# Optimization experiments

Hardware: AMD Instinct MI355X
Metric: run time of the kernel (lower is better)

## Reference

```python
import jax, jax.numpy as jnp
import numpy as np

N = 50000      # nodes
E = 800000     # edges (avg degree 16)
IN = 128       # in_channels
OUT = 128      # out_channels


def setup_inputs() -> dict:
    key = jax.random.key(0)
    k1, k2, k3 = jax.random.split(key, 3)
    x = jax.random.normal(k1, (N, IN), dtype=jnp.float32)
    edge_index = jax.random.randint(k2, (2, E), 0, N, dtype=jnp.int32)
    # GCNConv params: glorot-ish linear weight + zero bias
    W = jax.random.normal(k3, (IN, OUT), dtype=jnp.float32) / np.float32(np.sqrt(IN))
    b = jnp.zeros((OUT,), dtype=jnp.float32)
    return {"x": x, "W": W, "b": b, "edge_index": edge_index}


def reference(x, W, b, edge_index):
    n = x.shape[0]
    src, dst = edge_index[0], edge_index[1]
    # add self loops (GCNConv default add_self_loops=True)
    loop = jnp.arange(n, dtype=edge_index.dtype)
    src = jnp.concatenate([src, loop])
    dst = jnp.concatenate([dst, loop])
    # symmetric normalization: deg^{-1/2}[src] * deg^{-1/2}[dst], deg from dst (flow source_to_target)
    deg = jax.ops.segment_sum(jnp.ones_like(dst, dtype=x.dtype), dst, num_segments=n)
    dinv = jnp.where(deg > 0, jax.lax.rsqrt(jnp.maximum(deg, 1.0)), 0.0)
    norm = dinv[src] * dinv[dst]                     # [E+N]
    xw = x @ W                                       # [N, OUT] dense GEMM first (as GCNConv does)
    msg = xw[src] * norm[:, None]                    # [E+N, OUT] gather + scale
    out = jax.ops.segment_sum(msg, dst, num_segments=n)  # scatter-add aggregate
    return out + b
```

## Files before the change

### kernel.cpp

```cpp
#include <hip/hip_runtime.h>


constexpr int CH = 128;
constexpr int CHUNK = 4096;
constexpr int NCMAX = 256;

typedef __attribute__((ext_vector_type(8))) short short8;
typedef __attribute__((ext_vector_type(4))) float f32x4;

static __device__ __forceinline__ ushort f2bf(float f) {
    unsigned u = __float_as_uint(f);
    u += 0x7fff + ((u >> 16) & 1);
    return (ushort)(u >> 16);
}


__global__ __launch_bounds__(256) void hist_kernel(const int* __restrict__ dst,
                                                   int* __restrict__ h, int E, int nc) {
    __shared__ int hh[NCMAX];
    int t = threadIdx.x, b = blockIdx.x;
    for (int i = t; i < nc; i += 256) hh[i] = 0;
    __syncthreads();
    int s = b * CHUNK, e = min(E, s + CHUNK);
    for (int i = s + t; i < e; i += 256) atomicAdd(&hh[dst[i] >> 8], 1);
    __syncthreads();
    for (int i = t; i < nc; i += 256) h[b * nc + i] = hh[i];
}

__global__ __launch_bounds__(256) void colscan_cols(int* __restrict__ h,
        int* __restrict__ coltot, int nblk, int nc) {
    __shared__ int sm[256];
    int i = blockIdx.x;
    int t = threadIdx.x;
    int v = (t < nblk) ? h[t * nc + i] : 0;
    sm[t] = v;
    __syncthreads();
    #pragma unroll
    for (int d = 1; d < 256; d <<= 1) {
        int u = (t >= d) ? sm[t - d] : 0;
        __syncthreads();
        sm[t] += u;
        __syncthreads();
    }
    if (t < nblk) h[t * nc + i] = sm[t] - v;
    if (t == 255) coltot[i] = sm[255];
}

__global__ __launch_bounds__(256) void scan_bbase(const int* __restrict__ coltot,
        int* __restrict__ bbase, int nc) {
    __shared__ int sm[256];
    int t = threadIdx.x;
    int v = (t < nc) ? coltot[t] : 0;
    sm[t] = v;
    __syncthreads();
    #pragma unroll
    for (int d = 1; d < 256; d <<= 1) {
        int u = (t >= d) ? sm[t - d] : 0;
        __syncthreads();
        sm[t] += u;
        __syncthreads();
    }
    if (t < nc) bbase[t] = sm[t] - v;
    if (t == nc - 1) bbase[nc] = sm[t];
}

__global__ __launch_bounds__(256) void binscatter_kernel(const int* __restrict__ src,
        const int* __restrict__ dst, const int* __restrict__ h,
        const int* __restrict__ bbase, uint2* __restrict__ ebuf, int E, int nc) {
    __shared__ int cur[NCMAX];
    int t = threadIdx.x, b = blockIdx.x;
    for (int i = t; i < nc; i += 256) cur[i] = h[b * nc + i] + bbase[i];
    __syncthreads();
    int s = b * CHUNK, e = min(E, s + CHUNK);
    for (int i = s + t; i < e; i += 256) {
        int d = dst[i];
        int pos = atomicAdd(&cur[d >> 8], 1);
        ebuf[pos] = make_uint2((unsigned)src[i], (unsigned)d);
    }
}

__global__ __launch_bounds__(256) void bucket_csr_kernel(const uint2* __restrict__ ebuf,
        const int* __restrict__ bbase, int* __restrict__ off, int* __restrict__ csr,
        float* __restrict__ dinv, int N) {
    __shared__ int hist[256], cur[256], sc[256];
    int t = threadIdx.x, k = blockIdx.x;
    int s = bbase[k], e = bbase[k + 1];
    hist[t] = 0;
    __syncthreads();
    for (int i = s + t; i < e; i += 256) atomicAdd(&hist[ebuf[i].y & 255], 1);
    __syncthreads();
    int v = hist[t];
    sc[t] = v;
    __syncthreads();
    #pragma unroll
    for (int d = 1; d < 256; d <<= 1) {
        int u = (t >= d) ? sc[t - d] : 0;
        __syncthreads();
        sc[t] += u;
        __syncthreads();
    }
    int excl = sc[t] - v;
    int node = k * 256 + t;
    if (node <= N) off[node] = s + excl;
    if (node < N) dinv[node] = rsqrtf((float)(v + 1));
    cur[t] = s + excl;
    __syncthreads();
    for (int i = s + t; i < e; i += 256) {
        uint2 u = ebuf[i];
        int pos = atomicAdd(&cur[u.y & 255], 1);
        csr[pos] = (int)u.x;
    }
}


__global__ void pack_w(const float* __restrict__ W, ushort* __restrict__ Wp) {
    int tid = blockIdx.x * blockDim.x + threadIdx.x;
    if (tid >= 2048) return;
    int col = tid >> 4, chunk = tid & 15;
    ushort tmp[8];
    #pragma unroll
    for (int i = 0; i < 8; ++i)
        tmp[i] = f2bf(W[(size_t)(chunk * 8 + i) * CH + col]);
    int d = col * 16 + (chunk ^ (col & 7));
    *(uint4*)&Wp[(size_t)d * 8] = *(uint4*)tmp;
}


__global__ __launch_bounds__(256) void gemm_mfma(const float* __restrict__ x,
        const ushort* __restrict__ Wp, const float* __restrict__ dinv,
        ushort* __restrict__ xwd, int N) {
    __shared__ alignas(16) ushort Wlds[16384];
    int t = threadIdx.x;
    int wv = t >> 6, l = t & 63;
    int c15 = l & 15, kc = l >> 4;
    int row0 = blockIdx.x * 64 + wv * 16;
    int r = row0 + c15;
    bool valid = r < N;

    short8 af[4];
    #pragma unroll
    for (int ks = 0; ks < 4; ++ks) {
        float4 a0 = make_float4(0.f,0.f,0.f,0.f), a1 = a0;
        if (valid) {
            const float* p = x + (size_t)r * CH + ks * 32 + kc * 8;
            a0 = *(const float4*)p;
            a1 = *(const float4*)(p + 4);
        }
        short8 v;
        v[0]=f2bf(a0.x); v[1]=f2bf(a0.y); v[2]=f2bf(a0.z); v[3]=f2bf(a0.w);
        v[4]=f2bf(a1.x); v[5]=f2bf(a1.y); v[6]=f2bf(a1.z); v[7]=f2bf(a1.w);
        af[ks] = v;
    }

    #pragma unroll
    for (int i = 0; i < 8; ++i) {
        int idx = i * 256 + t;
        *(uint4*)&Wlds[idx * 8] = *(const uint4*)&Wp[idx * 8];
    }
    __syncthreads();

    f32x4 acc[8];
    #pragma unroll
    for (int ct = 0; ct < 8; ++ct) { f32x4 z = {0.f,0.f,0.f,0.f}; acc[ct] = z; }

    int swz = l & 7;
    #pragma unroll
    for (int ks = 0; ks < 4; ++ks) {
        #pragma unroll
        for (int ct = 0; ct < 8; ++ct) {
            int col = ct * 16 + c15;
            int idx16 = (col * 16 + ks * 4 + kc) ^ swz;
            short8 bfrag = *(const short8*)&Wlds[idx16 * 8];
            acc[ct] = __builtin_amdgcn_mfma_f32_16x16x32_bf16(af[ks], bfrag, acc[ct], 0, 0, 0);
        }
    }

    float dv[4];
    #pragma unroll
    for (int rr = 0; rr < 4; ++rr) {
        int row = row0 + kc * 4 + rr;
        dv[rr] = (row < N) ? dinv[row] : 0.f;
    }
    __syncthreads();

    ushort* bw = Wlds + wv * 2048;
    #pragma unroll
    for (int ct = 0; ct < 8; ++ct) {
        #pragma unroll
        for (int rr = 0; rr < 4; ++rr) {
            int row_local = kc * 4 + rr;
            bw[row_local * CH + ct * 16 + c15] = f2bf(acc[ct][rr] * dv[rr]);
        }
    }
    #pragma unroll
    for (int p = 0; p < 4; ++p) {
        int row_local = p * 4 + kc;
        int row = row0 + row_local;
        if (row < N) {
            uint4 vv = *(const uint4*)&bw[row_local * CH + c15 * 8];
            *(uint4*)&xwd[(size_t)row * CH + c15 * 8] = vv;
        }
    }
}


__global__ __launch_bounds__(256) void agg_kernel(const ushort* __restrict__ xwd,
        const int* __restrict__ csr, const int* __restrict__ off,
        const float* __restrict__ dinv, const float* __restrict__ b,
        float* __restrict__ out, int N) {
    int t = threadIdx.x;
    int c15 = t & 15;
    int node = blockIdx.x * 16 + (t >> 4);
    if (node >= N) return;
    int s = off[node], e = off[node + 1];
    float acc[8] = {0.f,0.f,0.f,0.f,0.f,0.f,0.f,0.f};
    const ushort* base = xwd + c15 * 8;

    int sr = (s < e) ? csr[s] : node;
    for (int j = s; j < e; ++j) {
        int nsr = (j + 1 < e) ? csr[j + 1] : node;
        uint4 v = *(const uint4*)(base + (size_t)sr * CH);
        acc[0] += __uint_as_float(v.x << 16);
        acc[1] += __uint_as_float(v.x & 0xffff0000u);
        acc[2] += __uint_as_float(v.y << 16);
        acc[3] += __uint_as_float(v.y & 0xffff0000u);
        acc[4] += __uint_as_float(v.z << 16);
        acc[5] += __uint_as_float(v.z & 0xffff0000u);
        acc[6] += __uint_as_float(v.w << 16);
        acc[7] += __uint_as_float(v.w & 0xffff0000u);
        sr = nsr;
    }
    {
        uint4 v = *(const uint4*)(base + (size_t)node * CH);
        acc[0] += __uint_as_float(v.x << 16);
        acc[1] += __uint_as_float(v.x & 0xffff0000u);
        acc[2] += __uint_as_float(v.y << 16);
        acc[3] += __uint_as_float(v.y & 0xffff0000u);
        acc[4] += __uint_as_float(v.z << 16);
        acc[5] += __uint_as_float(v.z & 0xffff0000u);
        acc[6] += __uint_as_float(v.w << 16);
        acc[7] += __uint_as_float(v.w & 0xffff0000u);
    }
    float di = dinv[node];
    float4 b0 = *(const float4*)&b[c15 * 8];
    float4 b1 = *(const float4*)&b[c15 * 8 + 4];
    float4 o0, o1;
    o0.x = di * acc[0] + b0.x;  o0.y = di * acc[1] + b0.y;
    o0.z = di * acc[2] + b0.z;  o0.w = di * acc[3] + b0.w;
    o1.x = di * acc[4] + b1.x;  o1.y = di * acc[5] + b1.y;
    o1.z = di * acc[6] + b1.z;  o1.w = di * acc[7] + b1.w;
    float* op = out + (size_t)node * CH + c15 * 8;
    *(float4*)op = o0;
    *(float4*)(op + 4) = o1;
}


extern "C" void kernel_launch(void* const* d_in, const int* in_sizes, int n_in,
                              void* d_out, int out_size, void* d_ws, size_t ws_size,
                              hipStream_t stream) {
    const float* x  = (const float*)d_in[0];
    const float* Wm = (const float*)d_in[1];
    const float* b  = (const float*)d_in[2];
    const int*   ei = (const int*)d_in[3];
    int N = in_sizes[0] / CH;
    int E = in_sizes[3] / 2;
    const int* src = ei;
    const int* dst = ei + E;
    float* out = (float*)d_out;

    char* w = (char*)d_ws;
    auto alloc = [&](size_t bytes) {
        char* p = w;
        w += (bytes + 255) & ~(size_t)255;
        return p;
    };
    int nc = (N + 255) >> 8;
    int nblk = (E + CHUNK - 1) / CHUNK;

    ushort* xwd  = (ushort*)alloc((size_t)N * CH * 2);
    uint2*  ebuf = (uint2*)xwd;
    int*    off  = (int*)alloc((size_t)(N + 1) * 4);
    int*    csr  = (int*)alloc((size_t)E * 4);
    float*  dinv = (float*)alloc((size_t)N * 4);
    ushort* Wp   = (ushort*)alloc((size_t)16384 * 2);
    int*    h    = (int*)alloc((size_t)nblk * nc * 4);
    int*    bbase= (int*)alloc((size_t)(nc + 1) * 4);
    int*    coltot=(int*)alloc((size_t)nc * 4);

    hist_kernel<<<nblk, 256, 0, stream>>>(dst, h, E, nc);
    colscan_cols<<<nc, 256, 0, stream>>>(h, coltot, nblk, nc);
    scan_bbase<<<1, 256, 0, stream>>>(coltot, bbase, nc);
    binscatter_kernel<<<nblk, 256, 0, stream>>>(src, dst, h, bbase, ebuf, E, nc);
    bucket_csr_kernel<<<nc, 256, 0, stream>>>(ebuf, bbase, off, csr, dinv, N);
    pack_w<<<8, 256, 0, stream>>>(Wm, Wp);
    gemm_mfma<<<(N + 63) / 64, 256, 0, stream>>>(x, Wp, dinv, xwd, N);
    agg_kernel<<<(N + 15) / 16, 256, 0, stream>>>(xwd, csr, off, dinv, b, out, N);
}
```

Baseline: 95.00 us.

## Pack edge indices into 16 bits and unroll aggregation gather loop by four

```diff
diff --git a/kernel.cpp b/kernel.cpp
--- a/kernel.cpp
+++ b/kernel.cpp
@@ -66,7 +66,7 @@
 
 __global__ __launch_bounds__(256) void binscatter_kernel(const int* __restrict__ src,
         const int* __restrict__ dst, const int* __restrict__ h,
-        const int* __restrict__ bbase, uint2* __restrict__ ebuf, int E, int nc) {
+        const int* __restrict__ bbase, unsigned* __restrict__ ebuf, int E, int nc) {
     __shared__ int cur[NCMAX];
     int t = threadIdx.x, b = blockIdx.x;
     for (int i = t; i < nc; i += 256) cur[i] = h[b * nc + i] + bbase[i];
@@ -75,19 +75,19 @@
     for (int i = s + t; i < e; i += 256) {
         int d = dst[i];
         int pos = atomicAdd(&cur[d >> 8], 1);
-        ebuf[pos] = make_uint2((unsigned)src[i], (unsigned)d);
-    }
-}
-
-__global__ __launch_bounds__(256) void bucket_csr_kernel(const uint2* __restrict__ ebuf,
-        const int* __restrict__ bbase, int* __restrict__ off, int* __restrict__ csr,
+        ebuf[pos] = (unsigned)src[i] | ((unsigned)(d & 255) << 16);
+    }
+}
+
+__global__ __launch_bounds__(256) void bucket_csr_kernel(const unsigned* __restrict__ ebuf,
+        const int* __restrict__ bbase, int* __restrict__ off, ushort* __restrict__ csr,
         float* __restrict__ dinv, int N) {
     __shared__ int hist[256], cur[256], sc[256];
     int t = threadIdx.x, k = blockIdx.x;
     int s = bbase[k], e = bbase[k + 1];
     hist[t] = 0;
     __syncthreads();
-    for (int i = s + t; i < e; i += 256) atomicAdd(&hist[ebuf[i].y & 255], 1);
+    for (int i = s + t; i < e; i += 256) atomicAdd(&hist[(ebuf[i] >> 16) & 255], 1);
     __syncthreads();
     int v = hist[t];
     sc[t] = v;
@@ -106,9 +106,9 @@
     cur[t] = s + excl;
     __syncthreads();
     for (int i = s + t; i < e; i += 256) {
-        uint2 u = ebuf[i];
-        int pos = atomicAdd(&cur[u.y & 255], 1);
-        csr[pos] = (int)u.x;
+        unsigned u = ebuf[i];
+        int pos = atomicAdd(&cur[(u >> 16) & 255], 1);
+        csr[pos] = (ushort)(u & 0xffffu);
     }
 }
 
@@ -204,8 +204,18 @@
 }
 
 
+#define ACC8(v)                                    \
+    acc[0] += __uint_as_float((v).x << 16);        \
+    acc[1] += __uint_as_float((v).x & 0xffff0000u);\
+    acc[2] += __uint_as_float((v).y << 16);        \
+    acc[3] += __uint_as_float((v).y & 0xffff0000u);\
+    acc[4] += __uint_as_float((v).z << 16);        \
+    acc[5] += __uint_as_float((v).z & 0xffff0000u);\
+    acc[6] += __uint_as_float((v).w << 16);        \
+    acc[7] += __uint_as_float((v).w & 0xffff0000u);
+
 __global__ __launch_bounds__(256) void agg_kernel(const ushort* __restrict__ xwd,
-        const int* __restrict__ csr, const int* __restrict__ off,
+        const ushort* __restrict__ csr, const int* __restrict__ off,
         const float* __restrict__ dinv, const float* __restrict__ b,
         float* __restrict__ out, int N) {
     int t = threadIdx.x;
@@ -216,30 +226,23 @@
     float acc[8] = {0.f,0.f,0.f,0.f,0.f,0.f,0.f,0.f};
     const ushort* base = xwd + c15 * 8;
 
-    int sr = (s < e) ? csr[s] : node;
-    for (int j = s; j < e; ++j) {
-        int nsr = (j + 1 < e) ? csr[j + 1] : node;
-        uint4 v = *(const uint4*)(base + (size_t)sr * CH);
-        acc[0] += __uint_as_float(v.x << 16);
-        acc[1] += __uint_as_float(v.x & 0xffff0000u);
-        acc[2] += __uint_as_float(v.y << 16);
-        acc[3] += __uint_as_float(v.y & 0xffff0000u);
-        acc[4] += __uint_as_float(v.z << 16);
-        acc[5] += __uint_as_float(v.z & 0xffff0000u);
-        acc[6] += __uint_as_float(v.w << 16);
-        acc[7] += __uint_as_float(v.w & 0xffff0000u);
-        sr = nsr;
+    int j = s;
+    for (; j + 4 <= e; j += 4) {
+        int i0 = csr[j], i1 = csr[j + 1], i2 = csr[j + 2], i3 = csr[j + 3];
+        uint4 v0 = *(const uint4*)(base + (size_t)i0 * CH);
+        uint4 v1 = *(const uint4*)(base + (size_t)i1 * CH);
+        uint4 v2 = *(const uint4*)(base + (size_t)i2 * CH);
+        uint4 v3 = *(const uint4*)(base + (size_t)i3 * CH);
+        ACC8(v0); ACC8(v1); ACC8(v2); ACC8(v3);
+    }
+    for (; j < e; ++j) {
+        int i0 = csr[j];
+        uint4 v = *(const uint4*)(base + (size_t)i0 * CH);
+        ACC8(v);
     }
     {
         uint4 v = *(const uint4*)(base + (size_t)node * CH);
-        acc[0] += __uint_as_float(v.x << 16);
-        acc[1] += __uint_as_float(v.x & 0xffff0000u);
-        acc[2] += __uint_as_float(v.y << 16);
-        acc[3] += __uint_as_float(v.y & 0xffff0000u);
-        acc[4] += __uint_as_float(v.z << 16);
-        acc[5] += __uint_as_float(v.z & 0xffff0000u);
-        acc[6] += __uint_as_float(v.w << 16);
-        acc[7] += __uint_as_float(v.w & 0xffff0000u);
+        ACC8(v);
     }
     float di = dinv[node];
     float4 b0 = *(const float4*)&b[c15 * 8];
@@ -277,15 +280,15 @@
     int nc = (N + 255) >> 8;
     int nblk = (E + CHUNK - 1) / CHUNK;
 
-    ushort* xwd  = (ushort*)alloc((size_t)N * CH * 2);
-    uint2*  ebuf = (uint2*)xwd;
-    int*    off  = (int*)alloc((size_t)(N + 1) * 4);
-    int*    csr  = (int*)alloc((size_t)E * 4);
-    float*  dinv = (float*)alloc((size_t)N * 4);
-    ushort* Wp   = (ushort*)alloc((size_t)16384 * 2);
-    int*    h    = (int*)alloc((size_t)nblk * nc * 4);
-    int*    bbase= (int*)alloc((size_t)(nc + 1) * 4);
-    int*    coltot=(int*)alloc((size_t)nc * 4);
+    ushort*   xwd  = (ushort*)alloc((size_t)N * CH * 2);
+    unsigned* ebuf = (unsigned*)xwd;
+    int*      off  = (int*)alloc((size_t)(N + 1) * 4);
+    ushort*   csr  = (ushort*)alloc((size_t)E * 2);
+    float*    dinv = (float*)alloc((size_t)N * 4);
+    ushort*   Wp   = (ushort*)alloc((size_t)16384 * 2);
+    int*      h    = (int*)alloc((size_t)nblk * nc * 4);
+    int*      bbase= (int*)alloc((size_t)(nc + 1) * 4);
+    int*      coltot=(int*)alloc((size_t)nc * 4);
 
     hist_kernel<<<nblk, 256, 0, stream>>>(dst, h, E, nc);
     colscan_cols<<<nc, 256, 0, stream>>>(h, coltot, nblk, nc);
```

New measurement: 83.43 us. 1.14x faster.
